# Kernel optimization log

Hardware: AMD Instinct MI355X
Metric: run time of the kernel (lower is better)

## Reference

```python
import jax, jax.numpy as jnp
import numpy as np

EMBED = 1024
HEAD = 64
CTX = 2048


def setup_inputs() -> dict:
    key = jax.random.key(0)
    ks = jax.random.split(key, 7)
    scale = 1.0 / np.sqrt(EMBED)
    return {
        "x": jax.random.normal(ks[0], (8, CTX, EMBED), dtype=jnp.float32),
        "Wq": jax.random.normal(ks[1], (EMBED, HEAD), dtype=jnp.float32) * scale,
        "bq": jax.random.normal(ks[2], (HEAD,), dtype=jnp.float32) * 0.01,
        "Wk": jax.random.normal(ks[3], (EMBED, HEAD), dtype=jnp.float32) * scale,
        "bk": jax.random.normal(ks[4], (HEAD,), dtype=jnp.float32) * 0.01,
        "Wv": jax.random.normal(ks[5], (EMBED, HEAD), dtype=jnp.float32) * scale,
        "bv": jax.random.normal(ks[6], (HEAD,), dtype=jnp.float32) * 0.01,
    }


def reference(x, Wq, bq, Wk, bk, Wv, bv):
    # x: [B, T, E]
    q = x @ Wq + bq  # [B, T, H]
    k = x @ Wk + bk
    v = x @ Wv + bv
    scores = jnp.einsum("bqh,bkh->bqk", q, k) / jnp.sqrt(jnp.float32(HEAD))
    T = x.shape[1]
    causal = jnp.tril(jnp.ones((T, T), dtype=bool))
    scores = jnp.where(causal, scores, -jnp.inf)
    attn = jax.nn.softmax(scores, axis=-1)  # dropout=0.0 -> identity
    out = jnp.einsum("bqk,bkh->bqh", attn, v)
    return out
```

## Files before the change

### kernel.cpp

```cpp
#include <hip/hip_runtime.h>
#include <math.h>
#include <stdint.h>

#define BDIM 8
#define TDIM 2048
#define EDIM 1024
#define HDIM 64
#define NCHUNK 144

typedef short bf16x8 __attribute__((ext_vector_type(8)));
typedef float f32x4 __attribute__((ext_vector_type(4)));

__device__ __forceinline__ unsigned short f2bf(float f) {
    uint32_t u = __builtin_bit_cast(uint32_t, f);
    u += 0x7fffu + ((u >> 16) & 1u);
    return (unsigned short)(u >> 16);
}
__device__ __forceinline__ float bf2f(unsigned short s) {
    uint32_t u = ((uint32_t)s) << 16;
    return __builtin_bit_cast(float, u);
}

__global__ __launch_bounds__(256) void prep_w(
    const float* __restrict__ Wq, const float* __restrict__ Wk,
    const float* __restrict__ Wv,
    unsigned short* __restrict__ WqT, unsigned short* __restrict__ WkT,
    unsigned short* __restrict__ WvT)
{
    int id = blockIdx.x * 256 + threadIdx.x;
    int e = id >> 6, h = id & 63;
    int oi = h * EDIM + e;
    WqT[oi] = f2bf(Wq[id]);
    WkT[oi] = f2bf(Wk[id]);
    WvT[oi] = f2bf(Wv[id]);
}

__global__ __launch_bounds__(256) void proj_kernel(
    const float* __restrict__ x,
    const unsigned short* __restrict__ WqT, const unsigned short* __restrict__ WkT,
    const unsigned short* __restrict__ WvT,
    const float* __restrict__ bq, const float* __restrict__ bk,
    const float* __restrict__ bv,
    unsigned short* __restrict__ Qb, unsigned short* __restrict__ Kb,
    unsigned short* __restrict__ VbT)
{
    __shared__ unsigned short Xs[2][64][72];
    __shared__ unsigned short Wqs[2][64][72];
    __shared__ unsigned short Wks[2][64][72];
    __shared__ unsigned short Wvs[2][64][72];

    const int t = threadIdx.x;
    const int lane = t & 63, w = t >> 6, quad = lane >> 4, ln = lane & 15;
    const int row0 = blockIdx.x * 64;
    const int sr = t >> 2;
    const int sc = (t & 3) << 4;

    f32x4 accq[4], acck[4], accv[4];
#pragma unroll
    for (int j = 0; j < 4; ++j) {
        accq[j] = (f32x4)(0.f); acck[j] = (f32x4)(0.f); accv[j] = (f32x4)(0.f);
    }

    const float* xp0  = &x[(size_t)(row0 + sr) * EDIM + sc];
    const size_t wrow = (size_t)sr * EDIM + sc;

    {
        float4 x0 = *(const float4*)(xp0);
        float4 x1 = *(const float4*)(xp0 + 4);
        float4 x2 = *(const float4*)(xp0 + 8);
        float4 x3 = *(const float4*)(xp0 + 12);
        bf16x8 xb0, xb1;
        xb0[0]=(short)f2bf(x0.x); xb0[1]=(short)f2bf(x0.y); xb0[2]=(short)f2bf(x0.z); xb0[3]=(short)f2bf(x0.w);
        xb0[4]=(short)f2bf(x1.x); xb0[5]=(short)f2bf(x1.y); xb0[6]=(short)f2bf(x1.z); xb0[7]=(short)f2bf(x1.w);
        xb1[0]=(short)f2bf(x2.x); xb1[1]=(short)f2bf(x2.y); xb1[2]=(short)f2bf(x2.z); xb1[3]=(short)f2bf(x2.w);
        xb1[4]=(short)f2bf(x3.x); xb1[5]=(short)f2bf(x3.y); xb1[6]=(short)f2bf(x3.z); xb1[7]=(short)f2bf(x3.w);
        *(bf16x8*)&Xs[0][sr][sc]     = xb0;
        *(bf16x8*)&Xs[0][sr][sc + 8] = xb1;
        *(bf16x8*)&Wqs[0][sr][sc]     = *(const bf16x8*)&WqT[wrow];
        *(bf16x8*)&Wqs[0][sr][sc + 8] = *(const bf16x8*)&WqT[wrow + 8];
        *(bf16x8*)&Wks[0][sr][sc]     = *(const bf16x8*)&WkT[wrow];
        *(bf16x8*)&Wks[0][sr][sc + 8] = *(const bf16x8*)&WkT[wrow + 8];
        *(bf16x8*)&Wvs[0][sr][sc]     = *(const bf16x8*)&WvT[wrow];
        *(bf16x8*)&Wvs[0][sr][sc + 8] = *(const bf16x8*)&WvT[wrow + 8];
    }

    for (int kt = 0; kt < EDIM / 64; ++kt) {
        const int cur = kt & 1, nxt = cur ^ 1;

        float4 x0, x1, x2, x3;
        bf16x8 wq0, wq1, wk0, wk1, wv0, wv1;
        if (kt < 15) {
            const float* xp = xp0 + (kt + 1) * 64;
            x0 = *(const float4*)(xp);
            x1 = *(const float4*)(xp + 4);
            x2 = *(const float4*)(xp + 8);
            x3 = *(const float4*)(xp + 12);
            const size_t wo = wrow + (kt + 1) * 64;
            wq0 = *(const bf16x8*)&WqT[wo];
            wq1 = *(const bf16x8*)&WqT[wo + 8];
            wk0 = *(const bf16x8*)&WkT[wo];
            wk1 = *(const bf16x8*)&WkT[wo + 8];
            wv0 = *(const bf16x8*)&WvT[wo];
            wv1 = *(const bf16x8*)&WvT[wo + 8];
        }

        __syncthreads();

        bf16x8 xa0 = *(const bf16x8*)&Xs[cur][16 * w + ln][8 * quad];
        bf16x8 xa1 = *(const bf16x8*)&Xs[cur][16 * w + ln][32 + 8 * quad];
#pragma unroll
        for (int j = 0; j < 4; ++j) {
            bf16x8 w0, w1;
            w0 = *(const bf16x8*)&Wqs[cur][16 * j + ln][8 * quad];
            w1 = *(const bf16x8*)&Wqs[cur][16 * j + ln][32 + 8 * quad];
            accq[j] = __builtin_amdgcn_mfma_f32_16x16x32_bf16(xa0, w0, accq[j], 0, 0, 0);
            accq[j] = __builtin_amdgcn_mfma_f32_16x16x32_bf16(xa1, w1, accq[j], 0, 0, 0);
            w0 = *(const bf16x8*)&Wks[cur][16 * j + ln][8 * quad];
            w1 = *(const bf16x8*)&Wks[cur][16 * j + ln][32 + 8 * quad];
            acck[j] = __builtin_amdgcn_mfma_f32_16x16x32_bf16(xa0, w0, acck[j], 0, 0, 0);
            acck[j] = __builtin_amdgcn_mfma_f32_16x16x32_bf16(xa1, w1, acck[j], 0, 0, 0);
            w0 = *(const bf16x8*)&Wvs[cur][16 * j + ln][8 * quad];
            w1 = *(const bf16x8*)&Wvs[cur][16 * j + ln][32 + 8 * quad];
            accv[j] = __builtin_amdgcn_mfma_f32_16x16x32_bf16(xa0, w0, accv[j], 0, 0, 0);
            accv[j] = __builtin_amdgcn_mfma_f32_16x16x32_bf16(xa1, w1, accv[j], 0, 0, 0);
        }

        if (kt < 15) {
            bf16x8 xb0, xb1;
            xb0[0]=(short)f2bf(x0.x); xb0[1]=(short)f2bf(x0.y); xb0[2]=(short)f2bf(x0.z); xb0[3]=(short)f2bf(x0.w);
            xb0[4]=(short)f2bf(x1.x); xb0[5]=(short)f2bf(x1.y); xb0[6]=(short)f2bf(x1.z); xb0[7]=(short)f2bf(x1.w);
            xb1[0]=(short)f2bf(x2.x); xb1[1]=(short)f2bf(x2.y); xb1[2]=(short)f2bf(x2.z); xb1[3]=(short)f2bf(x2.w);
            xb1[4]=(short)f2bf(x3.x); xb1[5]=(short)f2bf(x3.y); xb1[6]=(short)f2bf(x3.z); xb1[7]=(short)f2bf(x3.w);
            *(bf16x8*)&Xs[nxt][sr][sc]     = xb0;
            *(bf16x8*)&Xs[nxt][sr][sc + 8] = xb1;
            *(bf16x8*)&Wqs[nxt][sr][sc]     = wq0;
            *(bf16x8*)&Wqs[nxt][sr][sc + 8] = wq1;
            *(bf16x8*)&Wks[nxt][sr][sc]     = wk0;
            *(bf16x8*)&Wks[nxt][sr][sc + 8] = wk1;
            *(bf16x8*)&Wvs[nxt][sr][sc]     = wv0;
            *(bf16x8*)&Wvs[nxt][sr][sc + 8] = wv1;
        }
    }

#pragma unroll
    for (int j = 0; j < 4; ++j) {
        int col = 16 * j + ln;
        float bqv = bq[col], bkv = bk[col], bvv = bv[col];
#pragma unroll
        for (int r = 0; r < 4; ++r) {
            size_t row = (size_t)(row0 + 16 * w + 4 * quad + r);
            Qb[row * HDIM + col] = f2bf(accq[j][r] + bqv);
            Kb[row * HDIM + col] = f2bf(acck[j][r] + bkv);
            int bb = (int)(row >> 11);
            int tr = (int)(row & 2047);
            VbT[((size_t)bb * HDIM + col) * TDIM + tr] = f2bf(accv[j][r] + bvv);
        }
    }
}

__global__ __launch_bounds__(256) void attn_partial(
    const unsigned short* __restrict__ Qb, const unsigned short* __restrict__ Kb,
    const unsigned short* __restrict__ VbT,
    unsigned short* __restrict__ PO, float* __restrict__ Pm, float* __restrict__ Pl)
{
    __shared__ unsigned short Ks[2][64][72];
    __shared__ unsigned short VsT[2][64][72];
    __shared__ unsigned short Ps[64][72];

    const int t = threadIdx.x;
    const int lane = t & 63, w = t >> 6, quad = lane >> 4, ln = lane & 15;
    const int f = blockIdx.x;
    const int b = blockIdx.y;

    int g = 0;
    while (f >= 2 * (g + 1) * (g + 2)) ++g;
    const int r_  = f - 2 * g * (g + 1);
    const int iq  = 4 * g + r_ / (g + 1);
    const int ch  = r_ % (g + 1);

    const int q0 = iq * 64;
    const size_t base = (size_t)b * TDIM * HDIM;
    const int sr = t >> 2;
    const int sc = (t & 3) << 4;

    const size_t qrow = base + (size_t)(q0 + 16 * w + ln) * HDIM;
    bf16x8 qa0 = *(const bf16x8*)&Qb[qrow + 8 * quad];
    bf16x8 qa1 = *(const bf16x8*)&Qb[qrow + 32 + 8 * quad];

    f32x4 od[4];
#pragma unroll
    for (int j = 0; j < 4; ++j) od[j] = (f32x4)(0.f);
    float mrow[4], lrow[4];
#pragma unroll
    for (int r = 0; r < 4; ++r) { mrow[r] = -INFINITY; lrow[r] = 0.f; }

    const float scale = 0.125f;
    const int jt0 = 4 * ch;
    int j1 = jt0 + 3; if (j1 > iq) j1 = iq;

    {
        size_t ko = base + (size_t)(jt0 * 64 + sr) * HDIM + sc;
        *(bf16x8*)&Ks[0][sr][sc]     = *(const bf16x8*)&Kb[ko];
        *(bf16x8*)&Ks[0][sr][sc + 8] = *(const bf16x8*)&Kb[ko + 8];
        const unsigned short* vrow =
            &VbT[((size_t)b * HDIM + sr) * TDIM + jt0 * 64 + sc];
        *(bf16x8*)&VsT[0][sr][sc]     = *(const bf16x8*)vrow;
        *(bf16x8*)&VsT[0][sr][sc + 8] = *(const bf16x8*)(vrow + 8);
    }

    for (int jt = jt0; jt <= j1; ++jt) {
        const int cur = (jt - jt0) & 1, nxt = cur ^ 1;

        bf16x8 kn0, kn1, vn0, vn1;
        if (jt < j1) {
            size_t ko = base + (size_t)((jt + 1) * 64 + sr) * HDIM + sc;
            kn0 = *(const bf16x8*)&Kb[ko];
            kn1 = *(const bf16x8*)&Kb[ko + 8];
            const unsigned short* vrow =
                &VbT[((size_t)b * HDIM + sr) * TDIM + (jt + 1) * 64 + sc];
            vn0 = *(const bf16x8*)vrow;
            vn1 = *(const bf16x8*)(vrow + 8);
        }

        __syncthreads();

        f32x4 s[4];
#pragma unroll
        for (int j = 0; j < 4; ++j) {
            bf16x8 kb0 = *(const bf16x8*)&Ks[cur][16 * j + ln][8 * quad];
            bf16x8 kb1 = *(const bf16x8*)&Ks[cur][16 * j + ln][32 + 8 * quad];
            s[j] = (f32x4)(0.f);
            s[j] = __builtin_amdgcn_mfma_f32_16x16x32_bf16(qa0, kb0, s[j], 0, 0, 0);
            s[j] = __builtin_amdgcn_mfma_f32_16x16x32_bf16(qa1, kb1, s[j], 0, 0, 0);
        }

        if (jt == iq) {
#pragma unroll
            for (int j = 0; j < 4; ++j) {
                int kg = jt * 64 + 16 * j + ln;
#pragma unroll
                for (int r = 0; r < 4; ++r) {
                    int qg = q0 + 16 * w + 4 * quad + r;
                    s[j][r] = (kg <= qg) ? s[j][r] * scale : -INFINITY;
                }
            }
        } else {
#pragma unroll
            for (int j = 0; j < 4; ++j)
#pragma unroll
                for (int r = 0; r < 4; ++r) s[j][r] *= scale;
        }

        float mx[4];
#pragma unroll
        for (int r = 0; r < 4; ++r)
            mx[r] = fmaxf(fmaxf(s[0][r], s[1][r]), fmaxf(s[2][r], s[3][r]));
#pragma unroll
        for (int d = 1; d < 16; d <<= 1)
#pragma unroll
            for (int r = 0; r < 4; ++r)
                mx[r] = fmaxf(mx[r], __shfl_xor(mx[r], d));

        float al[4], rs[4];
#pragma unroll
        for (int r = 0; r < 4; ++r) {
            float mn = fmaxf(mrow[r], mx[r]);
            al[r] = __expf(mrow[r] - mn);
            mrow[r] = mn;
            float p0 = __expf(s[0][r] - mn);
            float p1 = __expf(s[1][r] - mn);
            float p2 = __expf(s[2][r] - mn);
            float p3 = __expf(s[3][r] - mn);
            s[0][r] = p0; s[1][r] = p1; s[2][r] = p2; s[3][r] = p3;
            rs[r] = (p0 + p1) + (p2 + p3);
        }
#pragma unroll
        for (int d = 1; d < 16; d <<= 1)
#pragma unroll
            for (int r = 0; r < 4; ++r)
                rs[r] += __shfl_xor(rs[r], d);
#pragma unroll
        for (int r = 0; r < 4; ++r) lrow[r] = lrow[r] * al[r] + rs[r];

#pragma unroll
        for (int j = 0; j < 4; ++j)
#pragma unroll
            for (int r = 0; r < 4; ++r) {
                od[j][r] *= al[r];
                Ps[16 * w + 4 * quad + r][16 * j + ln] = f2bf(s[j][r]);
            }

        bf16x8 pa0 = *(const bf16x8*)&Ps[16 * w + ln][8 * quad];
        bf16x8 pa1 = *(const bf16x8*)&Ps[16 * w + ln][32 + 8 * quad];
#pragma unroll
        for (int j = 0; j < 4; ++j) {
            bf16x8 vb0 = *(const bf16x8*)&VsT[cur][16 * j + ln][8 * quad];
            bf16x8 vb1 = *(const bf16x8*)&VsT[cur][16 * j + ln][32 + 8 * quad];
            od[j] = __builtin_amdgcn_mfma_f32_16x16x32_bf16(pa0, vb0, od[j], 0, 0, 0);
            od[j] = __builtin_amdgcn_mfma_f32_16x16x32_bf16(pa1, vb1, od[j], 0, 0, 0);
        }

        if (jt < j1) {
            *(bf16x8*)&Ks[nxt][sr][sc]     = kn0;
            *(bf16x8*)&Ks[nxt][sr][sc + 8] = kn1;
            *(bf16x8*)&VsT[nxt][sr][sc]     = vn0;
            *(bf16x8*)&VsT[nxt][sr][sc + 8] = vn1;
        }
    }

    const size_t p = (size_t)b * NCHUNK + f;
#pragma unroll
    for (int j = 0; j < 4; ++j)
#pragma unroll
        for (int r = 0; r < 4; ++r)
            PO[p * 4096 + (size_t)(16 * w + 4 * quad + r) * 64 + 16 * j + ln] =
                f2bf(od[j][r]);
    if (ln == 0) {
#pragma unroll
        for (int r = 0; r < 4; ++r) {
            Pm[p * 64 + 16 * w + 4 * quad + r] = mrow[r];
            Pl[p * 64 + 16 * w + 4 * quad + r] = lrow[r];
        }
    }
}

__global__ __launch_bounds__(256) void attn_combine(
    const unsigned short* __restrict__ PO, const float* __restrict__ Pm,
    const float* __restrict__ Pl, float* __restrict__ out)
{
    const int iq = blockIdx.x, b = blockIdx.y;
    const int g = iq >> 2;
    const int nch = g + 1;
    const int fbase = 2 * g * (g + 1) + (iq - 4 * g) * (g + 1);
    const int t = threadIdx.x;
    const int row = t >> 2;
    const int c0 = (t & 3) << 4;
    const size_t pbase = (size_t)b * NCHUNK + fbase;

    float M = -INFINITY;
    for (int c = 0; c < nch; ++c)
        M = fmaxf(M, Pm[(pbase + c) * 64 + row]);

    float a[16];
#pragma unroll
    for (int i = 0; i < 16; ++i) a[i] = 0.f;
    float L = 0.f;
    for (int c = 0; c < nch; ++c) {
        size_t p = pbase + c;
        float sc = __expf(Pm[p * 64 + row] - M);
        L += sc * Pl[p * 64 + row];
        const unsigned short* po = &PO[p * 4096 + (size_t)row * 64 + c0];
        bf16x8 v0 = *(const bf16x8*)(po);
        bf16x8 v1 = *(const bf16x8*)(po + 8);
#pragma unroll
        for (int i = 0; i < 8; ++i) {
            a[i]     += sc * bf2f((unsigned short)v0[i]);
            a[8 + i] += sc * bf2f((unsigned short)v1[i]);
        }
    }
    float li = 1.f / L;
    float4 o0, o1, o2, o3;
    o0.x=a[0]*li;  o0.y=a[1]*li;  o0.z=a[2]*li;  o0.w=a[3]*li;
    o1.x=a[4]*li;  o1.y=a[5]*li;  o1.z=a[6]*li;  o1.w=a[7]*li;
    o2.x=a[8]*li;  o2.y=a[9]*li;  o2.z=a[10]*li; o2.w=a[11]*li;
    o3.x=a[12]*li; o3.y=a[13]*li; o3.z=a[14]*li; o3.w=a[15]*li;
    float* op = &out[((size_t)b * TDIM + (size_t)iq * 64 + row) * HDIM + c0];
    *(float4*)(op)      = o0;
    *(float4*)(op + 4)  = o1;
    *(float4*)(op + 8)  = o2;
    *(float4*)(op + 12) = o3;
}

extern "C" void kernel_launch(void* const* d_in, const int* in_sizes, int n_in,
                              void* d_out, int out_size, void* d_ws, size_t ws_size,
                              hipStream_t stream) {
    const float* x  = (const float*)d_in[0];
    const float* Wq = (const float*)d_in[1];
    const float* bq = (const float*)d_in[2];
    const float* Wk = (const float*)d_in[3];
    const float* bk = (const float*)d_in[4];
    const float* Wv = (const float*)d_in[5];
    const float* bv = (const float*)d_in[6];
    float* out = (float*)d_out;

    const size_t n = (size_t)BDIM * TDIM * HDIM;
    unsigned short* Qb  = (unsigned short*)d_ws;
    unsigned short* Kb  = Qb + n;
    unsigned short* VbT = Kb + n;
    unsigned short* WqT = VbT + n;
    unsigned short* WkT = WqT + (size_t)EDIM * HDIM;
    unsigned short* WvT = WkT + (size_t)EDIM * HDIM;
    unsigned short* PO  = WvT + (size_t)EDIM * HDIM;
    float* Pm = (float*)(PO + (size_t)BDIM * NCHUNK * 4096);
    float* Pl = Pm + (size_t)BDIM * NCHUNK * 64;

    prep_w<<<dim3(EDIM * HDIM / 256), 256, 0, stream>>>(Wq, Wk, Wv, WqT, WkT, WvT);
    proj_kernel<<<dim3(BDIM * TDIM / 64), 256, 0, stream>>>(
        x, WqT, WkT, WvT, bq, bk, bv, Qb, Kb, VbT);
    attn_partial<<<dim3(NCHUNK, BDIM), 256, 0, stream>>>(Qb, Kb, VbT, PO, Pm, Pl);
    attn_combine<<<dim3(TDIM / 64, BDIM), 256, 0, stream>>>(PO, Pm, Pl, out);
}
```

Before: 148.4 us.

## Pre-pack weights into MFMA fragment layout and load directly from global

```diff
diff --git a/kernel.cpp b/kernel.cpp
--- a/kernel.cpp
+++ b/kernel.cpp
@@ -23,31 +23,35 @@
 
 __global__ __launch_bounds__(256) void prep_w(
     const float* __restrict__ Wq, const float* __restrict__ Wk,
-    const float* __restrict__ Wv,
-    unsigned short* __restrict__ WqT, unsigned short* __restrict__ WkT,
-    unsigned short* __restrict__ WvT)
+    const float* __restrict__ Wv, unsigned short* __restrict__ Wpk)
 {
-    int id = blockIdx.x * 256 + threadIdx.x;
-    int e = id >> 6, h = id & 63;
-    int oi = h * EDIM + e;
-    WqT[oi] = f2bf(Wq[id]);
-    WkT[oi] = f2bf(Wk[id]);
-    WvT[oi] = f2bf(Wv[id]);
+    int n = blockIdx.x * 256 + threadIdx.x;
+    int lane = n & 63;
+    int j    = (n >> 6) & 3;
+    int kt   = (n >> 8) & 15;
+    int m    = n >> 12;
+    const float* W = (m == 0) ? Wq : (m == 1) ? Wk : Wv;
+    int ln = lane & 15, quad = lane >> 4;
+    int h = 16 * j + ln;
+
+    bf16x8 c0, c1;
+#pragma unroll
+    for (int c = 0; c < 8; ++c) {
+        c0[c] = (short)f2bf(W[(size_t)(kt * 64 +      8 * quad + c) * HDIM + h]);
+        c1[c] = (short)f2bf(W[(size_t)(kt * 64 + 32 + 8 * quad + c) * HDIM + h]);
+    }
+    *(bf16x8*)&Wpk[(size_t)n * 16]     = c0;
+    *(bf16x8*)&Wpk[(size_t)n * 16 + 8] = c1;
 }
 
 __global__ __launch_bounds__(256) void proj_kernel(
-    const float* __restrict__ x,
-    const unsigned short* __restrict__ WqT, const unsigned short* __restrict__ WkT,
-    const unsigned short* __restrict__ WvT,
+    const float* __restrict__ x, const unsigned short* __restrict__ Wpk,
     const float* __restrict__ bq, const float* __restrict__ bk,
     const float* __restrict__ bv,
     unsigned short* __restrict__ Qb, unsigned short* __restrict__ Kb,
     unsigned short* __restrict__ VbT)
 {
     __shared__ unsigned short Xs[2][64][72];
-    __shared__ unsigned short Wqs[2][64][72];
-    __shared__ unsigned short Wks[2][64][72];
-    __shared__ unsigned short Wvs[2][64][72];
 
     const int t = threadIdx.x;
     const int lane = t & 63, w = t >> 6, quad = lane >> 4, ln = lane & 15;
@@ -61,8 +65,7 @@
         accq[j] = (f32x4)(0.f); acck[j] = (f32x4)(0.f); accv[j] = (f32x4)(0.f);
     }
 
-    const float* xp0  = &x[(size_t)(row0 + sr) * EDIM + sc];
-    const size_t wrow = (size_t)sr * EDIM + sc;
+    const float* xp0 = &x[(size_t)(row0 + sr) * EDIM + sc];
 
     {
         float4 x0 = *(const float4*)(xp0);
@@ -76,32 +79,31 @@
         xb1[4]=(short)f2bf(x3.x); xb1[5]=(short)f2bf(x3.y); xb1[6]=(short)f2bf(x3.z); xb1[7]=(short)f2bf(x3.w);
         *(bf16x8*)&Xs[0][sr][sc]     = xb0;
         *(bf16x8*)&Xs[0][sr][sc + 8] = xb1;
-        *(bf16x8*)&Wqs[0][sr][sc]     = *(const bf16x8*)&WqT[wrow];
-        *(bf16x8*)&Wqs[0][sr][sc + 8] = *(const bf16x8*)&WqT[wrow + 8];
-        *(bf16x8*)&Wks[0][sr][sc]     = *(const bf16x8*)&WkT[wrow];
-        *(bf16x8*)&Wks[0][sr][sc + 8] = *(const bf16x8*)&WkT[wrow + 8];
-        *(bf16x8*)&Wvs[0][sr][sc]     = *(const bf16x8*)&WvT[wrow];
-        *(bf16x8*)&Wvs[0][sr][sc + 8] = *(const bf16x8*)&WvT[wrow + 8];
     }
 
     for (int kt = 0; kt < EDIM / 64; ++kt) {
         const int cur = kt & 1, nxt = cur ^ 1;
 
+        bf16x8 wf0[3][4], wf1[3][4];
+        {
+            const size_t wb = (size_t)kt * 4096 + (size_t)lane * 16;
+#pragma unroll
+            for (int m = 0; m < 3; ++m)
+#pragma unroll
+                for (int j = 0; j < 4; ++j) {
+                    const unsigned short* p =
+                        &Wpk[(size_t)m * 65536 + wb + (size_t)j * 1024];
+                    wf0[m][j] = *(const bf16x8*)p;
+                    wf1[m][j] = *(const bf16x8*)(p + 8);
+                }
+        }
         float4 x0, x1, x2, x3;
-        bf16x8 wq0, wq1, wk0, wk1, wv0, wv1;
         if (kt < 15) {
             const float* xp = xp0 + (kt + 1) * 64;
             x0 = *(const float4*)(xp);
             x1 = *(const float4*)(xp + 4);
             x2 = *(const float4*)(xp + 8);
             x3 = *(const float4*)(xp + 12);
-            const size_t wo = wrow + (kt + 1) * 64;
-            wq0 = *(const bf16x8*)&WqT[wo];
-            wq1 = *(const bf16x8*)&WqT[wo + 8];
-            wk0 = *(const bf16x8*)&WkT[wo];
-            wk1 = *(const bf16x8*)&WkT[wo + 8];
-            wv0 = *(const bf16x8*)&WvT[wo];
-            wv1 = *(const bf16x8*)&WvT[wo + 8];
         }
 
         __syncthreads();
@@ -110,19 +112,12 @@
         bf16x8 xa1 = *(const bf16x8*)&Xs[cur][16 * w + ln][32 + 8 * quad];
 #pragma unroll
         for (int j = 0; j < 4; ++j) {
-            bf16x8 w0, w1;
-            w0 = *(const bf16x8*)&Wqs[cur][16 * j + ln][8 * quad];
-            w1 = *(const bf16x8*)&Wqs[cur][16 * j + ln][32 + 8 * quad];
-            accq[j] = __builtin_amdgcn_mfma_f32_16x16x32_bf16(xa0, w0, accq[j], 0, 0, 0);
-            accq[j] = __builtin_amdgcn_mfma_f32_16x16x32_bf16(xa1, w1, accq[j], 0, 0, 0);
-            w0 = *(const bf16x8*)&Wks[cur][16 * j + ln][8 * quad];
-            w1 = *(const bf16x8*)&Wks[cur][16 * j + ln][32 + 8 * quad];
-            acck[j] = __builtin_amdgcn_mfma_f32_16x16x32_bf16(xa0, w0, acck[j], 0, 0, 0);
-            acck[j] = __builtin_amdgcn_mfma_f32_16x16x32_bf16(xa1, w1, acck[j], 0, 0, 0);
-            w0 = *(const bf16x8*)&Wvs[cur][16 * j + ln][8 * quad];
-            w1 = *(const bf16x8*)&Wvs[cur][16 * j + ln][32 + 8 * quad];
-            accv[j] = __builtin_amdgcn_mfma_f32_16x16x32_bf16(xa0, w0, accv[j], 0, 0, 0);
-            accv[j] = __builtin_amdgcn_mfma_f32_16x16x32_bf16(xa1, w1, accv[j], 0, 0, 0);
+            accq[j] = __builtin_amdgcn_mfma_f32_16x16x32_bf16(xa0, wf0[0][j], accq[j], 0, 0, 0);
+            accq[j] = __builtin_amdgcn_mfma_f32_16x16x32_bf16(xa1, wf1[0][j], accq[j], 0, 0, 0);
+            acck[j] = __builtin_amdgcn_mfma_f32_16x16x32_bf16(xa0, wf0[1][j], acck[j], 0, 0, 0);
+            acck[j] = __builtin_amdgcn_mfma_f32_16x16x32_bf16(xa1, wf1[1][j], acck[j], 0, 0, 0);
+            accv[j] = __builtin_amdgcn_mfma_f32_16x16x32_bf16(xa0, wf0[2][j], accv[j], 0, 0, 0);
+            accv[j] = __builtin_amdgcn_mfma_f32_16x16x32_bf16(xa1, wf1[2][j], accv[j], 0, 0, 0);
         }
 
         if (kt < 15) {
@@ -133,12 +128,6 @@
             xb1[4]=(short)f2bf(x3.x); xb1[5]=(short)f2bf(x3.y); xb1[6]=(short)f2bf(x3.z); xb1[7]=(short)f2bf(x3.w);
             *(bf16x8*)&Xs[nxt][sr][sc]     = xb0;
             *(bf16x8*)&Xs[nxt][sr][sc + 8] = xb1;
-            *(bf16x8*)&Wqs[nxt][sr][sc]     = wq0;
-            *(bf16x8*)&Wqs[nxt][sr][sc + 8] = wq1;
-            *(bf16x8*)&Wks[nxt][sr][sc]     = wk0;
-            *(bf16x8*)&Wks[nxt][sr][sc + 8] = wk1;
-            *(bf16x8*)&Wvs[nxt][sr][sc]     = wv0;
-            *(bf16x8*)&Wvs[nxt][sr][sc + 8] = wv1;
         }
     }
 
@@ -387,16 +376,14 @@
     unsigned short* Qb  = (unsigned short*)d_ws;
     unsigned short* Kb  = Qb + n;
     unsigned short* VbT = Kb + n;
-    unsigned short* WqT = VbT + n;
-    unsigned short* WkT = WqT + (size_t)EDIM * HDIM;
-    unsigned short* WvT = WkT + (size_t)EDIM * HDIM;
-    unsigned short* PO  = WvT + (size_t)EDIM * HDIM;
+    unsigned short* Wpk = VbT + n;
+    unsigned short* PO  = Wpk + (size_t)3 * EDIM * HDIM;
     float* Pm = (float*)(PO + (size_t)BDIM * NCHUNK * 4096);
     float* Pl = Pm + (size_t)BDIM * NCHUNK * 64;
 
-    prep_w<<<dim3(EDIM * HDIM / 256), 256, 0, stream>>>(Wq, Wk, Wv, WqT, WkT, WvT);
+    prep_w<<<dim3(48), 256, 0, stream>>>(Wq, Wk, Wv, Wpk);
     proj_kernel<<<dim3(BDIM * TDIM / 64), 256, 0, stream>>>(
-        x, WqT, WkT, WvT, bq, bk, bv, Qb, Kb, VbT);
+        x, Wpk, bq, bk, bv, Qb, Kb, VbT);
     attn_partial<<<dim3(NCHUNK, BDIM), 256, 0, stream>>>(Qb, Kb, VbT, PO, Pm, Pl);
     attn_combine<<<dim3(TDIM / 64, BDIM), 256, 0, stream>>>(PO, Pm, Pl, out);
 }
```

New measurement: 156.1 us. +5.2%, slower.
